# Performance work log

Hardware: AMD Instinct MI355X
Metric: run time of the kernel (lower is better)

The kernel has to match this reference:

```python
import jax, jax.numpy as jnp
import numpy as np

B, H, W = 2, 64, 64
D = 256  # in_channels
EPS = 1e-5


def conv2d(x, w, pad):
    # x: NCHW, w: OIHW
    return jax.lax.conv_general_dilated(
        x, w, window_strides=(1, 1), padding=[(pad, pad), (pad, pad)],
        dimension_numbers=("NCHW", "OIHW", "NCHW"))


def code_projection(X, codewords, scale):
    # X: [B, D, H, W]; codewords: [K, D]; scale: [D, K]
    b, d = X.shape[0], X.shape[1]
    x = X.reshape(b, d, -1).transpose(0, 2, 1)              # [B, N, D]
    # residual: [B, N, D, K] (large broadcast tensor, as in the original)
    residual = (x[:, :, :, None] - codewords.T[None, None]) * scale
    Q = jax.nn.softmax(-0.5 * jnp.sum(residual ** 2, axis=2), axis=-1)  # [B, N, K]
    Z_num = jnp.einsum("bnk,bndk->bdk", Q, residual)        # sum over N
    Z_ = Z_num / Q.sum(axis=1)[:, None, :]                  # [B, D, K]
    Z = Z_ / jnp.sqrt(jnp.sum(Z_ ** 2, axis=1, keepdims=True))  # L2 over D
    return Z, Q


def graph_conv(inp, weight, gamma, beta):
    # inp: [B, D, K]
    adj = jnp.einsum("bdk,bdl->bkl", inp, inp)              # input^T @ input
    support = jnp.einsum("ij,bjk->bik", weight, inp)        # weight @ input
    out = jnp.einsum("bdk,bkl->bdl", support, adj)          # support @ adj
    out = jax.nn.relu(out)
    # BatchNorm1d (training-mode batch stats over (B, K) per channel D)
    mean = out.mean(axis=(0, 2), keepdims=True)
    var = out.var(axis=(0, 2), keepdims=True)
    return gamma[None, :, None] * (out - mean) / jnp.sqrt(var + EPS) + beta[None, :, None]


def reproj(graph, Q, h, w):
    # graph: [B, D, K], Q: [B, N, K]
    x = jnp.einsum("bdk,bnk->bdn", graph, Q)
    return x.reshape(graph.shape[0], graph.shape[1], h, w)


def branch(c, conv_w, cw, sc, gcnw, g, bta, ext_w, h, w):
    z, q = code_projection(conv2d(c, conv_w, 1), cw, sc)
    z = graph_conv(z, gcnw, g, bta)
    return conv2d(reproj(z, q, h, w), ext_w, 0) + c


def setup_inputs() -> dict:
    key = jax.random.key(0)
    keys = iter(jax.random.split(key, 64))
    nk = lambda: next(keys)
    inp = {}
    inp["c3"] = jax.random.normal(nk(), (B, 512, H, W), jnp.float32)
    inp["c4"] = jax.random.normal(nk(), (B, 512, H, W), jnp.float32)
    inp["c5"] = jax.random.normal(nk(), (B, 512, H, W), jnp.float32)
    for name, K in [("32", 32), ("16", 16), ("8", 8)]:
        inp[f"conv{name}_w"] = jax.random.normal(nk(), (256, 512, 3, 3), jnp.float32) * 0.02
        std1 = 1.0 / np.sqrt(K * D)
        inp[f"cw{name}"] = jax.random.uniform(nk(), (K, D), jnp.float32, -std1, std1)
        inp[f"sc{name}"] = jax.random.uniform(nk(), (D, K), jnp.float32, -1.0, 0.0)
        stdv = 1.0 / np.sqrt(D)
        inp[f"gcnw{name}"] = jax.random.uniform(nk(), (D, D), jnp.float32, -stdv, stdv)
        inp[f"bng{name}"] = jax.random.uniform(nk(), (D,), jnp.float32, 0.5, 1.5)
        inp[f"bnb{name}"] = jax.random.normal(nk(), (D,), jnp.float32) * 0.1
        inp[f"ext{name}_w"] = jax.random.normal(nk(), (512, 256, 1, 1), jnp.float32) * 0.05
    inp["smooth_w"] = jax.random.normal(nk(), (512, 1536, 3, 3), jnp.float32) * 0.01
    inp["smg"] = jax.random.uniform(nk(), (512,), jnp.float32, 0.5, 1.5)
    inp["smb"] = jax.random.normal(nk(), (512,), jnp.float32) * 0.1
    return inp


def reference(c3, c4, c5,
              conv32_w, cw32, sc32, gcnw32, bng32, bnb32, ext32_w,
              conv16_w, cw16, sc16, gcnw16, bng16, bnb16, ext16_w,
              conv8_w, cw8, sc8, gcnw8, bng8, bnb8, ext8_w,
              smooth_w, smg, smb):
    h, w = c3.shape[2], c3.shape[3]
    x_32 = branch(c3, conv32_w, cw32, sc32, gcnw32, bng32, bnb32, ext32_w, h, w)
    x_16 = branch(c4, conv16_w, cw16, sc16, gcnw16, bng16, bnb16, ext16_w, h, w)
    x_8 = branch(c5, conv8_w, cw8, sc8, gcnw8, bng8, bnb8, ext8_w, h, w)
    out = jnp.concatenate([x_8, x_16, x_32], axis=1)        # [B, 1536, H, W]
    out = conv2d(out, smooth_w, 1)
    # BatchNorm2d (training-mode batch stats) + ReLU
    mean = out.mean(axis=(0, 2, 3), keepdims=True)
    var = out.var(axis=(0, 2, 3), keepdims=True)
    out = smg[None, :, None, None] * (out - mean) / jnp.sqrt(var + EPS) + smb[None, :, None, None]
    return jax.nn.relu(out)
```

## Files before the change

kernel.cpp:

```cpp
#include <hip/hip_runtime.h>
#include <hip/hip_bf16.h>
#include <math.h>

#define HWN 4096
#define DCH 256
#define EPSV 1e-5f

typedef unsigned short u16;
typedef __attribute__((ext_vector_type(8))) short short8b;
typedef __attribute__((ext_vector_type(4))) float fx4;
typedef __attribute__((ext_vector_type(8))) unsigned short u16x8;

static __device__ inline u16 f2bf(float f) {
  __hip_bfloat16 h = __float2bfloat16(f);
  return *reinterpret_cast<u16*>(&h);
}
static __device__ inline float bf2f(u16 u) {
  unsigned int v = ((unsigned int)u) << 16;
  return __uint_as_float(v);
}

__global__ __launch_bounds__(256) void t_chwc3_k(const float* __restrict__ i0p,
    const float* __restrict__ i1p, const float* __restrict__ i2p,
    u16* __restrict__ out) {
  __shared__ float tl[32][257];
  const int p0 = blockIdx.x * 256, cic = blockIdx.y;
  const int z = blockIdx.z;
  const int br = z >> 1, b = z & 1;
  const float* in = (br == 0) ? i0p : ((br == 1) ? i1p : i2p);
  const int t = threadIdx.x;
  const float* ip = in + ((size_t)(b * 512 + cic * 32)) * HWN + p0;
#pragma unroll
  for (int r = 0; r < 32; ++r) tl[r][t] = ip[(size_t)r * HWN + t];
  __syncthreads();
  u16* op = out + ((size_t)((z * 16 + cic)) * HWN + p0 + t) * 32;
#pragma unroll
  for (int g = 0; g < 4; ++g) {
    u16x8 o;
#pragma unroll
    for (int j = 0; j < 8; ++j) o[j] = f2bf(tl[g * 8 + j][t]);
    *reinterpret_cast<u16x8*>(op + g * 8) = o;
  }
}

template<int CIN, int COUT>
__global__ __launch_bounds__(256) void wpack_k(const float* __restrict__ w0,
    const float* __restrict__ w1, const float* __restrict__ w2,
    u16* __restrict__ wp) {
  constexpr int NCIC = CIN / 32, NCOG = COUT / 16;
  const int br = blockIdx.y;
  const float* w = (br == 0) ? w0 : ((br == 1) ? w1 : w2);
  u16* wpb = wp + (size_t)br * 9 * NCIC * NCOG * 512;
  const int cog = blockIdx.x % NCOG, cic = blockIdx.x / NCOG;
  __shared__ float ws_[16 * 32 * 9];
  const int t = threadIdx.x;
  const float* src = w + ((size_t)(cog * 16) * CIN + cic * 32) * 9;
  for (int i = t; i < 4608; i += 256) {
    int co = i / 288, r = i % 288;
    ws_[i] = src[(size_t)co * CIN * 9 + r];
  }
  __syncthreads();
  const size_t tapstride = (size_t)NCIC * NCOG * 512;
  const size_t base = ((size_t)cic * NCOG + cog) * 512;
#pragma unroll
  for (int tap = 0; tap < 9; ++tap) {
#pragma unroll
    for (int e0 = 0; e0 < 512; e0 += 256) {
      int e = e0 + t;
      int kg = e >> 7, m = (e >> 3) & 15, j = e & 7;
      wpb[tap * tapstride + base + e] = f2bf(ws_[m * 288 + (kg * 8 + j) * 9 + tap]);
    }
  }
}

template<int CIN, int COUT, int SPLIT, int COW, int WPE, bool BF16OUT>
__global__ __launch_bounds__(256, WPE) void convlds_k(
    const u16* __restrict__ xt, const u16* __restrict__ wp,
    void* __restrict__ outv) {
  constexpr int NCIC = CIN / 32;
  constexpr int NCO = COUT / COW;
  constexpr int NWT = COW / 16;
  constexpr int CICPS = NCIC / SPLIT;
  constexpr int NST = CICPS * 3;
  constexpr int TAPB = COW * 32;
  constexpr int WSH = TAPB / 4;
  constexpr int RNDS = WSH / 512;
  constexpr size_t OUTEL = (size_t)2 * COUT * HWN;
  __shared__ u16 bl[2][3 * TAPB];

  const int br = blockIdx.y;
  xt += (size_t)br * 2 * NCIC * HWN * 32;
  wp += (size_t)br * 9 * NCIC * (COUT / 16) * 512;

  int g = blockIdx.x;
  const int cpx = (int)gridDim.x >> 3;
  g = (g & 7) * cpx + (g >> 3);
  const int s = g / (32 * NCO);
  const int rem = g % (32 * NCO);
  const int rt = rem / NCO;
  const int cob = (rem % NCO) * COW;

  const int wv = threadIdx.x >> 6, lane = threadIdx.x & 63;
  const int row = rt * 4 + wv;
  const int b = row >> 6, h = row & 63;
  const int m = lane & 15, kg = lane >> 4;
  const int cic0 = s * CICPS;

  fx4 acc[4][NWT];
#pragma unroll
  for (int i = 0; i < 4; ++i)
#pragma unroll
    for (int jn = 0; jn < NWT; ++jn) acc[i][jn] = (fx4){0.f, 0.f, 0.f, 0.f};

  const short8b zero8 = (short8b){0, 0, 0, 0, 0, 0, 0, 0};
  const int lds_lane = wv * WSH + lane * 8;

  {
    const int cic = cic0, ty = 0;
#pragma unroll
    for (int t3 = 0; t3 < 3; ++t3) {
      const int tap = ty * 3 + t3;
      const u16* srcb = wp + (((size_t)tap * NCIC + cic) * (COUT / 16) + (cob >> 4)) * 512;
#pragma unroll
      for (int r = 0; r < RNDS; ++r) {
        u16x8 v = *reinterpret_cast<const u16x8*>(srcb + lds_lane + r * 512);
        *reinterpret_cast<u16x8*>(&bl[0][t3 * TAPB + lds_lane + r * 512]) = v;
      }
    }
  }
  __syncthreads();

#pragma unroll 1
  for (int st = 0; st < NST; ++st) {
    const int cur = st & 1;
    u16x8 stg[3][RNDS];
    const bool hasnext = (st + 1 < NST);
    if (hasnext) {
      const int cicn = cic0 + (st + 1) / 3, tyn = (st + 1) % 3;
#pragma unroll
      for (int t3 = 0; t3 < 3; ++t3) {
        const int tap = tyn * 3 + t3;
        const u16* srcb = wp + (((size_t)tap * NCIC + cicn) * (COUT / 16) + (cob >> 4)) * 512;
#pragma unroll
        for (int r = 0; r < RNDS; ++r)
          stg[t3][r] = *reinterpret_cast<const u16x8*>(srcb + lds_lane + r * 512);
      }
    }
    const int cic = cic0 + st / 3, ty = st % 3;
    const int hh = h + ty - 1;
    if ((unsigned)hh < 64u) {
      const u16* rowp = xt + ((size_t)(b * NCIC + cic)) * HWN * 32
                        + (size_t)hh * 2048 + kg * 8;
#pragma unroll
      for (int tx = 0; tx < 3; ++tx) {
        short8b a[4];
#pragma unroll
        for (int mt = 0; mt < 4; ++mt) {
          int wi = mt * 16 + m + tx - 1;
          bool ok = ((unsigned)wi < 64u);
          int wc = ok ? wi : 0;
          short8b v = *reinterpret_cast<const short8b*>(rowp + wc * 32);
          a[mt] = ok ? v : zero8;
        }
        short8b bb[NWT];
#pragma unroll
        for (int nt = 0; nt < NWT; ++nt)
          bb[nt] = *reinterpret_cast<const short8b*>(&bl[cur][tx * TAPB + nt * 512 + lane * 8]);
#pragma unroll
        for (int mt = 0; mt < 4; ++mt)
#pragma unroll
          for (int nt = 0; nt < NWT; ++nt)
            acc[mt][nt] = __builtin_amdgcn_mfma_f32_16x16x32_bf16(a[mt], bb[nt], acc[mt][nt], 0, 0, 0);
      }
    }
    if (hasnext) {
#pragma unroll
      for (int t3 = 0; t3 < 3; ++t3)
#pragma unroll
        for (int r = 0; r < RNDS; ++r)
          *reinterpret_cast<u16x8*>(&bl[cur ^ 1][t3 * TAPB + lds_lane + r * 512]) = stg[t3][r];
    }
    __syncthreads();
  }

#pragma unroll
  for (int mt = 0; mt < 4; ++mt)
#pragma unroll
    for (int nt = 0; nt < NWT; ++nt) {
      int co = cob + nt * 16 + m;
      size_t idx = ((size_t)(b * COUT + co)) * HWN + h * 64 + mt * 16 + kg * 4;
      if (BF16OUT) {
        u16* op = (u16*)outv + (size_t)(br * SPLIT + s) * OUTEL + idx;
        ushort4 o;
        o.x = f2bf(acc[mt][nt][0]); o.y = f2bf(acc[mt][nt][1]);
        o.z = f2bf(acc[mt][nt][2]); o.w = f2bf(acc[mt][nt][3]);
        *reinterpret_cast<ushort4*>(op) = o;
      } else {
        float* op = (float*)outv + (size_t)(br * SPLIT + s) * OUTEL + idx;
        *reinterpret_cast<fx4*>(op) = acc[mt][nt];
      }
    }
}

__global__ __launch_bounds__(256) void sreduce_bn_k(const u16* __restrict__ slab,
    float* __restrict__ dout, float* __restrict__ pstat) {
  const int o = blockIdx.x, b = blockIdx.y;
  const size_t el = (size_t)2 * 512 * HWN;
  const size_t base = ((size_t)(b * 512 + o)) * HWN;
  const int t = threadIdx.x;
  float s = 0.f, ss = 0.f;
#pragma unroll
  for (int i0 = t * 8; i0 < HWN; i0 += 256 * 8) {
    u16x8 v0 = *reinterpret_cast<const u16x8*>(slab + base + i0);
    u16x8 v1 = *reinterpret_cast<const u16x8*>(slab + el + base + i0);
    u16x8 v2 = *reinterpret_cast<const u16x8*>(slab + 2 * el + base + i0);
    u16x8 v3 = *reinterpret_cast<const u16x8*>(slab + 3 * el + base + i0);
    fx4 y0, y1;
#pragma unroll
    for (int j = 0; j < 4; ++j) {
      float y = (bf2f(v0[j]) + bf2f(v1[j])) + (bf2f(v2[j]) + bf2f(v3[j]));
      y0[j] = y; s += y; ss = fmaf(y, y, ss);
    }
#pragma unroll
    for (int j = 0; j < 4; ++j) {
      float y = (bf2f(v0[4 + j]) + bf2f(v1[4 + j])) + (bf2f(v2[4 + j]) + bf2f(v3[4 + j]));
      y1[j] = y; s += y; ss = fmaf(y, y, ss);
    }
    *reinterpret_cast<fx4*>(dout + base + i0) = y0;
    *reinterpret_cast<fx4*>(dout + base + i0 + 4) = y1;
  }
  __shared__ float rs[4], rss[4];
  for (int off = 32; off; off >>= 1) { s += __shfl_down(s, off); ss += __shfl_down(ss, off); }
  int lane = t & 63, wid = t >> 6;
  if (lane == 0) { rs[wid] = s; rss[wid] = ss; }
  __syncthreads();
  if (t == 0) {
    pstat[(b * 512 + o) * 2]     = rs[0] + rs[1] + rs[2] + rs[3];
    pstat[(b * 512 + o) * 2 + 1] = rss[0] + rss[1] + rss[2] + rss[3];
  }
}

__global__ __launch_bounds__(512) void bnfin_k(const float* __restrict__ pstat,
    float* __restrict__ stat) {
  const int o = threadIdx.x;
  float S  = pstat[o * 2] + pstat[(512 + o) * 2];
  float SS = pstat[o * 2 + 1] + pstat[(512 + o) * 2 + 1];
  float mean = S / (2 * HWN);
  float var  = SS / (2 * HWN) - mean * mean;
  stat[o] = mean;
  stat[512 + o] = 1.f / sqrtf(var + EPSV);
}

__global__ __launch_bounds__(256) void prep3_k(
    const float* __restrict__ sc0, const float* __restrict__ sc1, const float* __restrict__ sc2,
    const float* __restrict__ cw0, const float* __restrict__ cw1, const float* __restrict__ cw2,
    float2* __restrict__ AB, float* __restrict__ Ck) {
  const int br = blockIdx.y;
  const int K = 8 << br;
  const int k = blockIdx.x;
  if (k >= K) return;
  const float* sc = (br == 0) ? sc0 : ((br == 1) ? sc1 : sc2);
  const float* cw = (br == 0) ? cw0 : ((br == 1) ? cw1 : cw2);
  float2* ABb = AB + 2048 * ((1 << br) - 1);
  float* Ckb = Ck + 8 * ((1 << br) - 1);
  const int d = threadIdx.x;
  float s = sc[d * K + k];
  float a = s * s;
  float c = cw[k * DCH + d];
  ABb[d * K + k] = make_float2(a, c * a);
  float tt = c * s;
  tt = tt * tt;
  __shared__ float red[4];
  for (int off = 32; off; off >>= 1) tt += __shfl_down(tt, off);
  int lane = threadIdx.x & 63, wid = threadIdx.x >> 6;
  if (lane == 0) red[wid] = tt;
  __syncthreads();
  if (threadIdx.x == 0) Ckb[k] = red[0] + red[1] + red[2] + red[3];
}

template<int K>
static __device__ void score_body(int b, float* sm,
    const u16* __restrict__ s0p, const u16* __restrict__ s1p,
    float* __restrict__ Xout,
    const float2* __restrict__ AB, const float* __restrict__ Ck,
    float* __restrict__ Qt, float* __restrict__ Qsp) {
  const int lane = threadIdx.x & 63;
  const int g = threadIdx.x >> 6;
  const int n = blockIdx.x * 64 + lane;
  const size_t bbase = ((size_t)b * DCH) * HWN + n;
  float s_[K];
#pragma unroll
  for (int k = 0; k < K; ++k) s_[k] = 0.f;
  for (int d = g * 64; d < g * 64 + 64; ++d) {
    const size_t ofs = bbase + (size_t)d * HWN;
    float xv = bf2f(s0p[ofs]) + bf2f(s1p[ofs]);
    Xout[ofs] = xv;
    float x2 = xv * xv;
    float xm = -2.f * xv;
    const float2* abp = AB + d * K;
#pragma unroll
    for (int k = 0; k < K; ++k) {
      float2 ab = abp[k];
      s_[k] = fmaf(x2, ab.x, s_[k]);
      s_[k] = fmaf(xm, ab.y, s_[k]);
    }
  }
  float* smr = sm + (g * 64 + lane) * (K + 1);
#pragma unroll
  for (int k = 0; k < K; ++k) smr[k] = s_[k];
  __syncthreads();
  if (g == 0) {
    const float* r0 = sm + lane * (K + 1);
    const float* r1 = sm + (64 + lane) * (K + 1);
    const float* r2 = sm + (128 + lane) * (K + 1);
    const float* r3 = sm + (192 + lane) * (K + 1);
    float mx = -1e30f;
#pragma unroll
    for (int k = 0; k < K; ++k) {
      float v = (r0[k] + r1[k]) + (r2[k] + r3[k]);
      s_[k] = -0.5f * (v + Ck[k]);
      mx = fmaxf(mx, s_[k]);
    }
    float sum = 0.f;
#pragma unroll
    for (int k = 0; k < K; ++k) { float e = expf(s_[k] - mx); s_[k] = e; sum += e; }
    float inv = 1.f / sum;
#pragma unroll
    for (int k = 0; k < K; ++k) {
      float v = s_[k] * inv;
      Qt[((size_t)(b * K + k)) * HWN + n] = v;
      for (int off = 32; off; off >>= 1) v += __shfl_down(v, off);
      if (lane == 0) Qsp[((size_t)(b * K + k)) * 64 + blockIdx.x] = v;
    }
  }
}

__global__ __launch_bounds__(256) void score3_k(const u16* __restrict__ bslab,
    float* __restrict__ X3,
    const float2* __restrict__ AB3, const float* __restrict__ Ck3,
    float* __restrict__ Qt3, float* __restrict__ Qsp3) {
  __shared__ float sm[4 * 64 * 33];
  const int z = blockIdx.y, br = z >> 1, b = z & 1;
  const size_t XEL = (size_t)2 * DCH * HWN;
  const u16* s0 = bslab + (size_t)br * 2 * XEL;
  const u16* s1 = s0 + XEL;
  if (br == 0)
    score_body<8>(b, sm, s0, s1, X3, AB3, Ck3, Qt3, Qsp3);
  else if (br == 1)
    score_body<16>(b, sm, s0, s1, X3 + XEL, AB3 + 2048, Ck3 + 8, Qt3 + 65536, Qsp3 + 1024);
  else
    score_body<32>(b, sm, s0, s1, X3 + 2 * XEL, AB3 + 6144, Ck3 + 24, Qt3 + 196608, Qsp3 + 3072);
}

template<int K>
static __device__ void mmulp_body(int b, float* xs, float* pw,
    const float* __restrict__ X, const float* __restrict__ Qt,
    float* __restrict__ Mp) {
  const int d = blockIdx.x, nch = blockIdx.y;
  const int t = threadIdx.x;
  const float* xp = X + ((size_t)(b * DCH + d)) * HWN + nch * 512;
  xs[t] = xp[t]; xs[t + 256] = xp[t + 256];
  __syncthreads();
  const int lane = t & 63, wid = t >> 6;
#pragma unroll
  for (int k = 0; k < K; ++k) {
    const float* qp = Qt + ((size_t)(b * K + k)) * HWN + nch * 512;
    float s = fmaf(xs[t], qp[t], xs[t + 256] * qp[t + 256]);
    for (int off = 32; off; off >>= 1) s += __shfl_down(s, off);
    if (lane == 0) pw[wid * 33 + k] = s;
  }
  __syncthreads();
  if (t < K)
    Mp[(((size_t)(b * DCH + d)) * K + t) * 8 + nch] =
        (pw[t] + pw[33 + t]) + (pw[66 + t] + pw[99 + t]);
}

__global__ __launch_bounds__(256) void mmulp3_k(const float* __restrict__ X3,
    const float* __restrict__ Qt3, float* __restrict__ Mp3) {
  __shared__ float xs[512];
  __shared__ float pw[4 * 33];
  const int z = blockIdx.z, br = z >> 1, b = z & 1;
  const size_t XEL = (size_t)2 * DCH * HWN;
  if (br == 0)
    mmulp_body<8>(b, xs, pw, X3, Qt3, Mp3);
  else if (br == 1)
    mmulp_body<16>(b, xs, pw, X3 + XEL, Qt3 + 65536, Mp3 + 32768);
  else
    mmulp_body<32>(b, xs, pw, X3 + 2 * XEL, Qt3 + 196608, Mp3 + 98304);
}

template<int K>
static __device__ void fuse1_body(int b, float* buf, const float* __restrict__ Mp,
    const float* __restrict__ Qsp, const float* __restrict__ sc,
    const float* __restrict__ cw, const float* __restrict__ Wm,
    float* __restrict__ Graw) {
  float* zl = buf;
  float* adj = zl + DCH * K;
  float* rn = adj + K * K;
  float* qsl = rn + K;
  const int t = threadIdx.x;
  if (t < K) {
    const float* qp = Qsp + ((size_t)(b * K + t)) * 64;
    float s = 0.f;
    for (int i = 0; i < 64; ++i) s += qp[i];
    qsl[t] = s;
  }
  __syncthreads();
#pragma unroll
  for (int k = 0; k < K; ++k) {
    const float* mp = Mp + (((size_t)(b * DCH + t)) * K + k) * 8;
    fx4 p0 = *reinterpret_cast<const fx4*>(mp);
    fx4 p1 = *reinterpret_cast<const fx4*>(mp + 4);
    float mm = ((p0[0] + p0[1]) + (p0[2] + p0[3])) + ((p1[0] + p1[1]) + (p1[2] + p1[3]));
    float qs = qsl[k];
    zl[t * K + k] = sc[t * K + k] * (mm - cw[k * DCH + t] * qs) / qs;
  }
  __syncthreads();
  if (t < K) {
    float s = 0.f;
    for (int i = 0; i < DCH; ++i) { float v = zl[i * K + t]; s = fmaf(v, v, s); }
    rn[t] = 1.f / sqrtf(s);
  }
  __syncthreads();
#pragma unroll
  for (int k = 0; k < K; ++k) zl[t * K + k] *= rn[k];
  __syncthreads();
  for (int p = t; p < K * K; p += 256) {
    int k = p / K, l = p % K;
    float s = 0.f;
    for (int i = 0; i < DCH; ++i) s = fmaf(zl[i * K + k], zl[i * K + l], s);
    adj[p] = s;
  }
  __syncthreads();
  float sup[K];
#pragma unroll
  for (int k = 0; k < K; ++k) sup[k] = 0.f;
  const float* wr = Wm + (size_t)t * DCH;
  for (int jj = 0; jj < DCH; ++jj) {
    float wv = wr[jj];
#pragma unroll
    for (int k = 0; k < K; ++k) sup[k] = fmaf(wv, zl[jj * K + k], sup[k]);
  }
#pragma unroll
  for (int l = 0; l < K; ++l) {
    float s = 0.f;
#pragma unroll
    for (int k = 0; k < K; ++k) s = fmaf(sup[k], adj[k * K + l], s);
    Graw[((size_t)(b * DCH + t)) * K + l] = fmaxf(s, 0.f);
  }
}

__global__ __launch_bounds__(256) void fuse13_k(const float* __restrict__ Mp3,
    const float* __restrict__ Qsp3,
    const float* __restrict__ sc0, const float* __restrict__ sc1, const float* __restrict__ sc2,
    const float* __restrict__ cw0, const float* __restrict__ cw1, const float* __restrict__ cw2,
    const float* __restrict__ wm0, const float* __restrict__ wm1, const float* __restrict__ wm2,
    float* __restrict__ Graw3) {
  __shared__ float buf[DCH * 32 + 32 * 32 + 64];
  const int z = blockIdx.x, br = z >> 1, b = z & 1;
  if (br == 0)
    fuse1_body<8>(b, buf, Mp3, Qsp3, sc0, cw0, wm0, Graw3);
  else if (br == 1)
    fuse1_body<16>(b, buf, Mp3 + 32768, Qsp3 + 1024, sc1, cw1, wm1, Graw3 + 4096);
  else
    fuse1_body<32>(b, buf, Mp3 + 98304, Qsp3 + 3072, sc2, cw2, wm2, Graw3 + 12288);
}

template<int K>
static __device__ void fuse2_body(int b, int ob, float* gl,
    const float* __restrict__ Graw, const float* __restrict__ gamma,
    const float* __restrict__ beta, const float* __restrict__ E,
    float* __restrict__ EG) {
  const int t = threadIdx.x;
  {
    const int d = t;
    float s = 0.f, ss = 0.f;
#pragma unroll
    for (int b2 = 0; b2 < 2; ++b2)
#pragma unroll
      for (int l = 0; l < K; ++l) {
        float v = Graw[((size_t)(b2 * DCH + d)) * K + l];
        s += v; ss = fmaf(v, v, ss);
      }
    const float invn = 1.f / (2 * K);
    float mean = s * invn;
    float var  = ss * invn - mean * mean;
    float giv  = gamma[d] / sqrtf(var + EPSV);
    float be   = beta[d];
#pragma unroll
    for (int l = 0; l < K; ++l) {
      float v = Graw[((size_t)(b * DCH + d)) * K + l];
      gl[d * K + l] = fmaf(v - mean, giv, be);
    }
  }
  __syncthreads();
  const int o = ob * 256 + t;
  float a[K];
#pragma unroll
  for (int k = 0; k < K; ++k) a[k] = 0.f;
  const fx4* e4 = reinterpret_cast<const fx4*>(E + (size_t)o * DCH);
  for (int d4 = 0; d4 < 64; ++d4) {
    fx4 v = e4[d4];
#pragma unroll
    for (int j = 0; j < 4; ++j) {
      float vv = v[j];
#pragma unroll
      for (int k = 0; k < K; ++k)
        a[k] = fmaf(vv, gl[(d4 * 4 + j) * K + k], a[k]);
    }
  }
#pragma unroll
  for (int k = 0; k < K; ++k)
    EG[((size_t)(b * 512 + o)) * K + k] = a[k];
}

__global__ __launch_bounds__(256) void fuse23_k(const float* __restrict__ Graw3,
    const float* __restrict__ g0, const float* __restrict__ g1, const float* __restrict__ g2,
    const float* __restrict__ b0, const float* __restrict__ b1, const float* __restrict__ b2,
    const float* __restrict__ e0, const float* __restrict__ e1, const float* __restrict__ e2,
    float* __restrict__ EG3) {
  __shared__ float gl[DCH * 32];
  const int b = blockIdx.x, ob = blockIdx.y, br = blockIdx.z;
  if (br == 0)
    fuse2_body<8>(b, ob, gl, Graw3, g0, b0, e0, EG3);
  else if (br == 1)
    fuse2_body<16>(b, ob, gl, Graw3 + 4096, g1, b1, e1, EG3 + 8192);
  else
    fuse2_body<32>(b, ob, gl, Graw3 + 12288, g2, b2, e2, EG3 + 24576);
}

template<int K>
static __device__ void yout_body(int b, u16* egl, const float* __restrict__ EG,
    const float* __restrict__ Qt, const float* __restrict__ cres,
    u16* __restrict__ cat, int coff) {
  const int cg = blockIdx.y;
  const int t = threadIdx.x;
  const int lane = t & 63, sub = t >> 6;
  const int n = blockIdx.x * 64 + lane;
  for (int i = t; i < K * 128; i += 256) {
    int k = i >> 7, co = i & 127;
    egl[i] = f2bf(EG[((size_t)(b * 512 + cg * 128 + co)) * K + k]);
  }
  float q[K];
#pragma unroll
  for (int k = 0; k < K; ++k) q[k] = Qt[((size_t)(b * K + k)) * HWN + n];
  __syncthreads();
  const float* crow = cres + (size_t)b * 512 * HWN + n;
#pragma unroll
  for (int it = 0; it < 4; ++it) {
    int co = sub * 32 + it * 8;
    int gco = cg * 128 + co;
    float y[8];
#pragma unroll
    for (int jj = 0; jj < 8; ++jj) y[jj] = crow[(size_t)(gco + jj) * HWN];
#pragma unroll
    for (int k = 0; k < K; ++k) {
      u16x8 eg = *reinterpret_cast<const u16x8*>(&egl[k * 128 + co]);
#pragma unroll
      for (int jj = 0; jj < 8; ++jj) y[jj] = fmaf(bf2f(eg[jj]), q[k], y[jj]);
    }
    u16x8 o;
#pragma unroll
    for (int jj = 0; jj < 8; ++jj) o[jj] = f2bf(y[jj]);
    int ch = coff + gco;
    *reinterpret_cast<u16x8*>(cat +
        (((size_t)(b * 48 + (ch >> 5)) * HWN + n) * 32 + (ch & 31))) = o;
  }
}

__global__ __launch_bounds__(256) void yout3_k(const float* __restrict__ EG3,
    const float* __restrict__ Qt3, const float* __restrict__ c5,
    const float* __restrict__ c4, const float* __restrict__ c3,
    u16* __restrict__ cat) {
  __shared__ u16 egl[32 * 128];
  const int z = blockIdx.z, br = z >> 1, b = z & 1;
  if (br == 0)
    yout_body<8>(b, egl, EG3, Qt3, c5, cat, 0);
  else if (br == 1)
    yout_body<16>(b, egl, EG3 + 8192, Qt3 + 65536, c4, cat, 512);
  else
    yout_body<32>(b, egl, EG3 + 24576, Qt3 + 196608, c3, cat, 1024);
}

__global__ __launch_bounds__(256) void bnrelu_k(float* __restrict__ out,
    const float* __restrict__ stat, const float* __restrict__ g,
    const float* __restrict__ bb) {
  int idx = blockIdx.x * 256 + threadIdx.x;
  int o = (idx >> 12) & 511;
  float v = out[idx];
  float r = fmaf((v - stat[o]) * stat[512 + o], g[o], bb[o]);
  out[idx] = fmaxf(r, 0.f);
}

extern "C" void kernel_launch(void* const* d_in, const int* in_sizes, int n_in,
                              void* d_out, int out_size, void* d_ws, size_t ws_size,
                              hipStream_t stream) {
  const float* c3 = (const float*)d_in[0];
  const float* c4 = (const float*)d_in[1];
  const float* c5 = (const float*)d_in[2];
  const float* smooth_w = (const float*)d_in[24];
  const float* smg = (const float*)d_in[25];
  const float* smb = (const float*)d_in[26];
  float* dout = (float*)d_out;

  char* wsb = (char*)d_ws;
  u16* Xt3 = (u16*)wsb;
  u16* cat = (u16*)wsb;
  u16* Wb  = (u16*)(wsb + 25165824);
  float* stat  = (float*)(wsb + 39321600);
  float* pstat = (float*)(wsb + 39325696);
  float* pool  = (float*)(wsb + 39346176);
  char* C = wsb + 43540480;
  u16* bslab   = (u16*)C;
  float* X3    = (float*)(C + 25165824);
  u16* sslab   = (u16*)C;

  float* Qt3  = pool;
  float* Qsp3 = pool + 458752;
  float* Mp3  = pool + 465920;
  float* Graw3 = pool + 723968;
  float* EG3  = pool + 752640;
  float2* AB3 = (float2*)(pool + 809984);
  float* Ck3  = pool + 838656;

  t_chwc3_k<<<dim3(16, 16, 6), 256, 0, stream>>>(c5, c4, c3, Xt3);
  wpack_k<512, 256><<<dim3(256, 3), 256, 0, stream>>>(
      (const float*)d_in[17], (const float*)d_in[10], (const float*)d_in[3], Wb);
  convlds_k<512, 256, 2, 64, 3, true><<<dim3(256, 3), 256, 0, stream>>>(Xt3, Wb, bslab);

  prep3_k<<<dim3(32, 3), 256, 0, stream>>>(
      (const float*)d_in[19], (const float*)d_in[12], (const float*)d_in[5],
      (const float*)d_in[18], (const float*)d_in[11], (const float*)d_in[4],
      AB3, Ck3);
  score3_k<<<dim3(64, 6), 256, 0, stream>>>(bslab, X3, AB3, Ck3, Qt3, Qsp3);
  mmulp3_k<<<dim3(256, 8, 6), 256, 0, stream>>>(X3, Qt3, Mp3);
  fuse13_k<<<6, 256, 0, stream>>>(Mp3, Qsp3,
      (const float*)d_in[19], (const float*)d_in[12], (const float*)d_in[5],
      (const float*)d_in[18], (const float*)d_in[11], (const float*)d_in[4],
      (const float*)d_in[20], (const float*)d_in[13], (const float*)d_in[6],
      Graw3);
  fuse23_k<<<dim3(2, 2, 3), 256, 0, stream>>>(Graw3,
      (const float*)d_in[21], (const float*)d_in[14], (const float*)d_in[7],
      (const float*)d_in[22], (const float*)d_in[15], (const float*)d_in[8],
      (const float*)d_in[23], (const float*)d_in[16], (const float*)d_in[9],
      EG3);
  yout3_k<<<dim3(64, 4, 6), 256, 0, stream>>>(EG3, Qt3, c5, c4, c3, cat);

  wpack_k<1536, 512><<<dim3(1536, 1), 256, 0, stream>>>(smooth_w, smooth_w, smooth_w, Wb);
  convlds_k<1536, 512, 4, 128, 2, true><<<dim3(512, 1), 256, 0, stream>>>(cat, Wb, sslab);
  sreduce_bn_k<<<dim3(512, 2), 256, 0, stream>>>(sslab, dout, pstat);
  bnfin_k<<<1, 512, 0, stream>>>(pstat, stat);
  bnrelu_k<<<16384, 256, 0, stream>>>(dout, stat, smg, smb);
}
```

Before: 466.8 us.

## Stage conv input rows in LDS, fuse BN stats+apply, drop fp32 X copy

The conv kernel now stages six input rows per channel chunk (with zero halo) into LDS, shared across the four waves, instead of each wave reading global memory per tap. The weight buffer becomes single-buffered, with an extra barrier per stage. The final BN reduction, finalize and ReLU apply are fused into one kernel per channel that keeps values in registers, so the fp32 output is not read back. The score and mmulp kernels read the bf16 split slabs directly rather than a materialized fp32 X tensor. Together these cut global traffic and launches, at the cost of more LDS and lost double-buffering overlap in the conv.

```diff
diff --git a/kernel.cpp b/kernel.cpp
--- a/kernel.cpp
+++ b/kernel.cpp
@@ -74,7 +74,7 @@
 }
 
 template<int CIN, int COUT, int SPLIT, int COW, int WPE, bool BF16OUT>
-__global__ __launch_bounds__(256, WPE) void convlds_k(
+__global__ __launch_bounds__(256, WPE) void convlds2_k(
     const u16* __restrict__ xt, const u16* __restrict__ wp,
     void* __restrict__ outv) {
   constexpr int NCIC = CIN / 32;
@@ -85,8 +85,10 @@
   constexpr int TAPB = COW * 32;
   constexpr int WSH = TAPB / 4;
   constexpr int RNDS = WSH / 512;
+  constexpr int AROW = 66 * 32;
   constexpr size_t OUTEL = (size_t)2 * COUT * HWN;
-  __shared__ u16 bl[2][3 * TAPB];
+  __shared__ u16 bl[3 * TAPB];
+  __shared__ u16 al[6 * AROW];
 
   const int br = blockIdx.y;
   xt += (size_t)br * 2 * NCIC * HWN * 32;
@@ -101,10 +103,12 @@
   const int cob = (rem % NCO) * COW;
 
   const int wv = threadIdx.x >> 6, lane = threadIdx.x & 63;
-  const int row = rt * 4 + wv;
-  const int b = row >> 6, h = row & 63;
+  const int b = (rt * 4) >> 6;
+  const int h0 = (rt * 4) & 63;
+  const int h = h0 + wv;
   const int m = lane & 15, kg = lane >> 4;
   const int cic0 = s * CICPS;
+  const int t = threadIdx.x;
 
   fx4 acc[4][NWT];
 #pragma unroll
@@ -112,29 +116,42 @@
 #pragma unroll
     for (int jn = 0; jn < NWT; ++jn) acc[i][jn] = (fx4){0.f, 0.f, 0.f, 0.f};
 
-  const short8b zero8 = (short8b){0, 0, 0, 0, 0, 0, 0, 0};
+  const u16x8 zero16 = (u16x8){0, 0, 0, 0, 0, 0, 0, 0};
   const int lds_lane = wv * WSH + lane * 8;
 
+  auto stage_a = [&](int cic) {
+    const u16* xc = xt + ((size_t)(b * NCIC + cic)) * HWN * 32;
+#pragma unroll
+    for (int r = 0; r < 6; ++r) {
+      const int hl = h0 - 1 + r;
+      u16x8 v = zero16;
+      if ((unsigned)hl < 64u)
+        v = *reinterpret_cast<const u16x8*>(xc + (size_t)hl * 2048 + t * 8);
+      *reinterpret_cast<u16x8*>(&al[r * AROW + 32 + t * 8]) = v;
+    }
+    if (t < 48) {
+      int r = t >> 3, side = (t >> 2) & 1, part = t & 3;
+      *reinterpret_cast<u16x8*>(&al[r * AROW + (side ? 65 * 32 : 0) + part * 8]) = zero16;
+    }
+  };
+
+  stage_a(cic0);
   {
-    const int cic = cic0, ty = 0;
 #pragma unroll
     for (int t3 = 0; t3 < 3; ++t3) {
-      const int tap = ty * 3 + t3;
-      const u16* srcb = wp + (((size_t)tap * NCIC + cic) * (COUT / 16) + (cob >> 4)) * 512;
-#pragma unroll
-      for (int r = 0; r < RNDS; ++r) {
-        u16x8 v = *reinterpret_cast<const u16x8*>(srcb + lds_lane + r * 512);
-        *reinterpret_cast<u16x8*>(&bl[0][t3 * TAPB + lds_lane + r * 512]) = v;
-      }
+      const u16* srcb = wp + (((size_t)t3 * NCIC + cic0) * (COUT / 16) + (cob >> 4)) * 512;
+#pragma unroll
+      for (int r = 0; r < RNDS; ++r)
+        *reinterpret_cast<u16x8*>(&bl[t3 * TAPB + lds_lane + r * 512]) =
+            *reinterpret_cast<const u16x8*>(srcb + lds_lane + r * 512);
     }
   }
   __syncthreads();
 
 #pragma unroll 1
   for (int st = 0; st < NST; ++st) {
-    const int cur = st & 1;
+    const bool hasnext = (st + 1 < NST);
     u16x8 stg[3][RNDS];
-    const bool hasnext = (st + 1 < NST);
     if (hasnext) {
       const int cicn = cic0 + (st + 1) / 3, tyn = (st + 1) % 3;
 #pragma unroll
@@ -146,41 +163,34 @@
           stg[t3][r] = *reinterpret_cast<const u16x8*>(srcb + lds_lane + r * 512);
       }
     }
-    const int cic = cic0 + st / 3, ty = st % 3;
-    const int hh = h + ty - 1;
-    if ((unsigned)hh < 64u) {
-      const u16* rowp = xt + ((size_t)(b * NCIC + cic)) * HWN * 32
-                        + (size_t)hh * 2048 + kg * 8;
-#pragma unroll
-      for (int tx = 0; tx < 3; ++tx) {
-        short8b a[4];
-#pragma unroll
-        for (int mt = 0; mt < 4; ++mt) {
-          int wi = mt * 16 + m + tx - 1;
-          bool ok = ((unsigned)wi < 64u);
-          int wc = ok ? wi : 0;
-          short8b v = *reinterpret_cast<const short8b*>(rowp + wc * 32);
-          a[mt] = ok ? v : zero8;
-        }
-        short8b bb[NWT];
+    const int ty = st % 3;
+    const u16* arow = al + (wv + ty) * AROW + kg * 8;
+#pragma unroll
+    for (int tx = 0; tx < 3; ++tx) {
+      short8b a[4];
+#pragma unroll
+      for (int mt = 0; mt < 4; ++mt)
+        a[mt] = *reinterpret_cast<const short8b*>(arow + (mt * 16 + m + tx) * 32);
+      short8b bb[NWT];
+#pragma unroll
+      for (int nt = 0; nt < NWT; ++nt)
+        bb[nt] = *reinterpret_cast<const short8b*>(&bl[tx * TAPB + nt * 512 + lane * 8]);
+#pragma unroll
+      for (int mt = 0; mt < 4; ++mt)
 #pragma unroll
         for (int nt = 0; nt < NWT; ++nt)
-          bb[nt] = *reinterpret_cast<const short8b*>(&bl[cur][tx * TAPB + nt * 512 + lane * 8]);
-#pragma unroll
-        for (int mt = 0; mt < 4; ++mt)
-#pragma unroll
-          for (int nt = 0; nt < NWT; ++nt)
-            acc[mt][nt] = __builtin_amdgcn_mfma_f32_16x16x32_bf16(a[mt], bb[nt], acc[mt][nt], 0, 0, 0);
-      }
-    }
+          acc[mt][nt] = __builtin_amdgcn_mfma_f32_16x16x32_bf16(a[mt], bb[nt], acc[mt][nt], 0, 0, 0);
+    }
+    __syncthreads();
     if (hasnext) {
+      if (ty == 2) stage_a(cic0 + (st + 1) / 3);
 #pragma unroll
       for (int t3 = 0; t3 < 3; ++t3)
 #pragma unroll
         for (int r = 0; r < RNDS; ++r)
-          *reinterpret_cast<u16x8*>(&bl[cur ^ 1][t3 * TAPB + lds_lane + r * 512]) = stg[t3][r];
-    }
-    __syncthreads();
+          *reinterpret_cast<u16x8*>(&bl[t3 * TAPB + lds_lane + r * 512]) = stg[t3][r];
+      __syncthreads();
+    }
   }
 
 #pragma unroll
@@ -202,53 +212,59 @@
     }
 }
 
-__global__ __launch_bounds__(256) void sreduce_bn_k(const u16* __restrict__ slab,
-    float* __restrict__ dout, float* __restrict__ pstat) {
-  const int o = blockIdx.x, b = blockIdx.y;
+__global__ __launch_bounds__(256) void bnall_k(const u16* __restrict__ slab,
+    float* __restrict__ dout, const float* __restrict__ gm,
+    const float* __restrict__ bt) {
+  const int o = blockIdx.x;
   const size_t el = (size_t)2 * 512 * HWN;
-  const size_t base = ((size_t)(b * 512 + o)) * HWN;
-  const int t = threadIdx.x;
+  const int t = threadIdx.x;
+  float y[2][2][8];
   float s = 0.f, ss = 0.f;
 #pragma unroll
-  for (int i0 = t * 8; i0 < HWN; i0 += 256 * 8) {
-    u16x8 v0 = *reinterpret_cast<const u16x8*>(slab + base + i0);
-    u16x8 v1 = *reinterpret_cast<const u16x8*>(slab + el + base + i0);
-    u16x8 v2 = *reinterpret_cast<const u16x8*>(slab + 2 * el + base + i0);
-    u16x8 v3 = *reinterpret_cast<const u16x8*>(slab + 3 * el + base + i0);
-    fx4 y0, y1;
-#pragma unroll
-    for (int j = 0; j < 4; ++j) {
-      float y = (bf2f(v0[j]) + bf2f(v1[j])) + (bf2f(v2[j]) + bf2f(v3[j]));
-      y0[j] = y; s += y; ss = fmaf(y, y, ss);
-    }
-#pragma unroll
-    for (int j = 0; j < 4; ++j) {
-      float y = (bf2f(v0[4 + j]) + bf2f(v1[4 + j])) + (bf2f(v2[4 + j]) + bf2f(v3[4 + j]));
-      y1[j] = y; s += y; ss = fmaf(y, y, ss);
-    }
-    *reinterpret_cast<fx4*>(dout + base + i0) = y0;
-    *reinterpret_cast<fx4*>(dout + base + i0 + 4) = y1;
-  }
-  __shared__ float rs[4], rss[4];
+  for (int b = 0; b < 2; ++b)
+#pragma unroll
+    for (int c = 0; c < 2; ++c) {
+      const size_t base = ((size_t)(b * 512 + o)) * HWN + c * 2048 + t * 8;
+      u16x8 v0 = *reinterpret_cast<const u16x8*>(slab + base);
+      u16x8 v1 = *reinterpret_cast<const u16x8*>(slab + el + base);
+      u16x8 v2 = *reinterpret_cast<const u16x8*>(slab + 2 * el + base);
+      u16x8 v3 = *reinterpret_cast<const u16x8*>(slab + 3 * el + base);
+#pragma unroll
+      for (int j = 0; j < 8; ++j) {
+        float yv = (bf2f(v0[j]) + bf2f(v1[j])) + (bf2f(v2[j]) + bf2f(v3[j]));
+        y[b][c][j] = yv; s += yv; ss = fmaf(yv, yv, ss);
+      }
+    }
+  __shared__ float rs[4], rss[4], fin[2];
   for (int off = 32; off; off >>= 1) { s += __shfl_down(s, off); ss += __shfl_down(ss, off); }
   int lane = t & 63, wid = t >> 6;
   if (lane == 0) { rs[wid] = s; rss[wid] = ss; }
   __syncthreads();
   if (t == 0) {
-    pstat[(b * 512 + o) * 2]     = rs[0] + rs[1] + rs[2] + rs[3];
-    pstat[(b * 512 + o) * 2 + 1] = rss[0] + rss[1] + rss[2] + rss[3];
-  }
-}
-
-__global__ __launch_bounds__(512) void bnfin_k(const float* __restrict__ pstat,
-    float* __restrict__ stat) {
-  const int o = threadIdx.x;
-  float S  = pstat[o * 2] + pstat[(512 + o) * 2];
-  float SS = pstat[o * 2 + 1] + pstat[(512 + o) * 2 + 1];
-  float mean = S / (2 * HWN);
-  float var  = SS / (2 * HWN) - mean * mean;
-  stat[o] = mean;
-  stat[512 + o] = 1.f / sqrtf(var + EPSV);
+    float S = rs[0] + rs[1] + rs[2] + rs[3];
+    float SS = rss[0] + rss[1] + rss[2] + rss[3];
+    float mean = S / (2 * HWN);
+    float var = SS / (2 * HWN) - mean * mean;
+    fin[0] = mean;
+    fin[1] = 1.f / sqrtf(var + EPSV);
+  }
+  __syncthreads();
+  const float mean = fin[0], giv = fin[1] * gm[o], be = bt[o];
+#pragma unroll
+  for (int b = 0; b < 2; ++b)
+#pragma unroll
+    for (int c = 0; c < 2; ++c) {
+      const size_t base = ((size_t)(b * 512 + o)) * HWN + c * 2048 + t * 8;
+      fx4 o0, o1;
+#pragma unroll
+      for (int j = 0; j < 4; ++j)
+        o0[j] = fmaxf(fmaf(y[b][c][j] - mean, giv, be), 0.f);
+#pragma unroll
+      for (int j = 0; j < 4; ++j)
+        o1[j] = fmaxf(fmaf(y[b][c][4 + j] - mean, giv, be), 0.f);
+      *reinterpret_cast<fx4*>(dout + base) = o0;
+      *reinterpret_cast<fx4*>(dout + base + 4) = o1;
+    }
 }
 
 __global__ __launch_bounds__(256) void prep3_k(
@@ -281,7 +297,6 @@
 template<int K>
 static __device__ void score_body(int b, float* sm,
     const u16* __restrict__ s0p, const u16* __restrict__ s1p,
-    float* __restrict__ Xout,
     const float2* __restrict__ AB, const float* __restrict__ Ck,
     float* __restrict__ Qt, float* __restrict__ Qsp) {
   const int lane = threadIdx.x & 63;
@@ -294,7 +309,6 @@
   for (int d = g * 64; d < g * 64 + 64; ++d) {
     const size_t ofs = bbase + (size_t)d * HWN;
     float xv = bf2f(s0p[ofs]) + bf2f(s1p[ofs]);
-    Xout[ofs] = xv;
     float x2 = xv * xv;
     float xm = -2.f * xv;
     const float2* abp = AB + d * K;
@@ -336,7 +350,6 @@
 }
 
 __global__ __launch_bounds__(256) void score3_k(const u16* __restrict__ bslab,
-    float* __restrict__ X3,
     const float2* __restrict__ AB3, const float* __restrict__ Ck3,
     float* __restrict__ Qt3, float* __restrict__ Qsp3) {
   __shared__ float sm[4 * 64 * 33];
@@ -345,21 +358,22 @@
   const u16* s0 = bslab + (size_t)br * 2 * XEL;
   const u16* s1 = s0 + XEL;
   if (br == 0)
-    score_body<8>(b, sm, s0, s1, X3, AB3, Ck3, Qt3, Qsp3);
+    score_body<8>(b, sm, s0, s1, AB3, Ck3, Qt3, Qsp3);
   else if (br == 1)
-    score_body<16>(b, sm, s0, s1, X3 + XEL, AB3 + 2048, Ck3 + 8, Qt3 + 65536, Qsp3 + 1024);
+    score_body<16>(b, sm, s0, s1, AB3 + 2048, Ck3 + 8, Qt3 + 65536, Qsp3 + 1024);
   else
-    score_body<32>(b, sm, s0, s1, X3 + 2 * XEL, AB3 + 6144, Ck3 + 24, Qt3 + 196608, Qsp3 + 3072);
+    score_body<32>(b, sm, s0, s1, AB3 + 6144, Ck3 + 24, Qt3 + 196608, Qsp3 + 3072);
 }
 
 template<int K>
 static __device__ void mmulp_body(int b, float* xs, float* pw,
-    const float* __restrict__ X, const float* __restrict__ Qt,
-    float* __restrict__ Mp) {
+    const u16* __restrict__ s0p, const u16* __restrict__ s1p,
+    const float* __restrict__ Qt, float* __restrict__ Mp) {
   const int d = blockIdx.x, nch = blockIdx.y;
   const int t = threadIdx.x;
-  const float* xp = X + ((size_t)(b * DCH + d)) * HWN + nch * 512;
-  xs[t] = xp[t]; xs[t + 256] = xp[t + 256];
+  const size_t ofs = ((size_t)(b * DCH + d)) * HWN + nch * 512 + t;
+  xs[t] = bf2f(s0p[ofs]) + bf2f(s1p[ofs]);
+  xs[t + 256] = bf2f(s0p[ofs + 256]) + bf2f(s1p[ofs + 256]);
   __syncthreads();
   const int lane = t & 63, wid = t >> 6;
 #pragma unroll
@@ -375,18 +389,20 @@
         (pw[t] + pw[33 + t]) + (pw[66 + t] + pw[99 + t]);
 }
 
-__global__ __launch_bounds__(256) void mmulp3_k(const float* __restrict__ X3,
+__global__ __launch_bounds__(256) void mmulp3_k(const u16* __restrict__ bslab,
     const float* __restrict__ Qt3, float* __restrict__ Mp3) {
   __shared__ float xs[512];
   __shared__ float pw[4 * 33];
   const int z = blockIdx.z, br = z >> 1, b = z & 1;
   const size_t XEL = (size_t)2 * DCH * HWN;
+  const u16* s0 = bslab + (size_t)br * 2 * XEL;
+  const u16* s1 = s0 + XEL;
   if (br == 0)
-    mmulp_body<8>(b, xs, pw, X3, Qt3, Mp3);
+    mmulp_body<8>(b, xs, pw, s0, s1, Qt3, Mp3);
   else if (br == 1)
-    mmulp_body<16>(b, xs, pw, X3 + XEL, Qt3 + 65536, Mp3 + 32768);
+    mmulp_body<16>(b, xs, pw, s0, s1, Qt3 + 65536, Mp3 + 32768);
   else
-    mmulp_body<32>(b, xs, pw, X3 + 2 * XEL, Qt3 + 196608, Mp3 + 98304);
+    mmulp_body<32>(b, xs, pw, s0, s1, Qt3 + 196608, Mp3 + 98304);
 }
 
 template<int K>
@@ -582,16 +598,6 @@
     yout_body<32>(b, egl, EG3 + 24576, Qt3 + 196608, c3, cat, 1024);
 }
 
-__global__ __launch_bounds__(256) void bnrelu_k(float* __restrict__ out,
-    const float* __restrict__ stat, const float* __restrict__ g,
-    const float* __restrict__ bb) {
-  int idx = blockIdx.x * 256 + threadIdx.x;
-  int o = (idx >> 12) & 511;
-  float v = out[idx];
-  float r = fmaf((v - stat[o]) * stat[512 + o], g[o], bb[o]);
-  out[idx] = fmaxf(r, 0.f);
-}
-
 extern "C" void kernel_launch(void* const* d_in, const int* in_sizes, int n_in,
                               void* d_out, int out_size, void* d_ws, size_t ws_size,
                               hipStream_t stream) {
@@ -607,12 +613,9 @@
   u16* Xt3 = (u16*)wsb;
   u16* cat = (u16*)wsb;
   u16* Wb  = (u16*)(wsb + 25165824);
-  float* stat  = (float*)(wsb + 39321600);
-  float* pstat = (float*)(wsb + 39325696);
-  float* pool  = (float*)(wsb + 39346176);
+  float* pool  = (float*)(wsb + 39321600);
   char* C = wsb + 43540480;
   u16* bslab   = (u16*)C;
-  float* X3    = (float*)(C + 25165824);
   u16* sslab   = (u16*)C;
 
   float* Qt3  = pool;
@@ -626,14 +629,14 @@
   t_chwc3_k<<<dim3(16, 16, 6), 256, 0, stream>>>(c5, c4, c3, Xt3);
   wpack_k<512, 256><<<dim3(256, 3), 256, 0, stream>>>(
       (const float*)d_in[17], (const float*)d_in[10], (const float*)d_in[3], Wb);
-  convlds_k<512, 256, 2, 64, 3, true><<<dim3(256, 3), 256, 0, stream>>>(Xt3, Wb, bslab);
+  convlds2_k<512, 256, 2, 64, 3, true><<<dim3(256, 3), 256, 0, stream>>>(Xt3, Wb, bslab);
 
   prep3_k<<<dim3(32, 3), 256, 0, stream>>>(
       (const float*)d_in[19], (const float*)d_in[12], (const float*)d_in[5],
       (const float*)d_in[18], (const float*)d_in[11], (const float*)d_in[4],
       AB3, Ck3);
-  score3_k<<<dim3(64, 6), 256, 0, stream>>>(bslab, X3, AB3, Ck3, Qt3, Qsp3);
-  mmulp3_k<<<dim3(256, 8, 6), 256, 0, stream>>>(X3, Qt3, Mp3);
+  score3_k<<<dim3(64, 6), 256, 0, stream>>>(bslab, AB3, Ck3, Qt3, Qsp3);
+  mmulp3_k<<<dim3(256, 8, 6), 256, 0, stream>>>(bslab, Qt3, Mp3);
   fuse13_k<<<6, 256, 0, stream>>>(Mp3, Qsp3,
       (const float*)d_in[19], (const float*)d_in[12], (const float*)d_in[5],
       (const float*)d_in[18], (const float*)d_in[11], (const float*)d_in[4],
@@ -647,8 +650,6 @@
   yout3_k<<<dim3(64, 4, 6), 256, 0, stream>>>(EG3, Qt3, c5, c4, c3, cat);
 
   wpack_k<1536, 512><<<dim3(1536, 1), 256, 0, stream>>>(smooth_w, smooth_w, smooth_w, Wb);
-  convlds_k<1536, 512, 4, 128, 2, true><<<dim3(512, 1), 256, 0, stream>>>(cat, Wb, sslab);
-  sreduce_bn_k<<<dim3(512, 2), 256, 0, stream>>>(sslab, dout, pstat);
-  bnfin_k<<<1, 512, 0, stream>>>(pstat, stat);
-  bnrelu_k<<<16384, 256, 0, stream>>>(dout, stat, smg, smb);
-}
+  convlds2_k<1536, 512, 4, 128, 2, true><<<dim3(512, 1), 256, 0, stream>>>(cat, Wb, sslab);
+  bnall_k<<<512, 256, 0, stream>>>(sslab, dout, smg, smb);
+}
```

Measured after the change: 425.2 us. 1.1x faster.
